# Optimization experiments

Measured on AMD Instinct MI355X. Metric: run time of the kernel, lower is better.

Reference implementation:

```python
import jax, jax.numpy as jnp
import numpy as np

KERNEL_SIZE = 15  # module init kwarg


def _box_filter(x, k):
    c = x.shape[1]
    dn = ('NCHW', 'OIHW', 'NCHW')
    kh = jnp.ones((c, 1, k, 1), x.dtype)
    kw = jnp.ones((c, 1, 1, k), x.dtype)
    p = k // 2
    x = jax.lax.conv_general_dilated(x, kh, (1, 1), [(p, p), (0, 0)],
                                     dimension_numbers=dn, feature_group_count=c)
    x = jax.lax.conv_general_dilated(x, kw, (1, 1), [(0, 0), (p, p)],
                                     dimension_numbers=dn, feature_group_count=c)
    return x


def setup_inputs() -> dict:
    key = jax.random.key(0)
    k1, k2 = jax.random.split(key)
    b, c, h, w = 8, 19, 512, 1024
    input = jax.random.normal(k1, (b, c, h, w), dtype=jnp.float32)
    target = jax.random.randint(k2, (b, 1, h, w), 0, c, dtype=jnp.int32)
    return {"input": input, "target": target}


def reference(input, target):
    k = KERNEL_SIZE
    c = input.shape[1]
    # one-hot mask [b,c,h,w] (equivalent to the per-class (target==i) cat loop)
    mask = jnp.transpose(jax.nn.one_hot(target[:, 0], c, dtype=input.dtype), (0, 3, 1, 2))
    # per-class local count of same-class pixels in a k x k window
    count = _box_filter(mask, k)
    # since mask is one-hot, sum over channels picks the count at the true class (>= 1)
    wsum = jnp.sum(count * mask, axis=1, keepdims=True)  # [b,1,h,w]
    weight = (k * k) / wsum
    # gather the input score at the true class and weight it
    out = jnp.sum(input * mask, axis=1, keepdims=True) * (-weight)
    return jnp.mean(out)
```

## Files before the change

kernel.cpp:

```cpp
#include <hip/hip_runtime.h>
#include <stdint.h>

#define BB 8
#define CC 19
#define HH 512
#define WW 1024
#define KK 15
#define RR 7
#define TH 8
#define NROWS (TH + 2*RR)
#define P_DW 34
#define HW (HH*WW)
#define NPIX (BB*HH*WW)
#define NBLK (BB*(HH/TH))

__global__ __launch_bounds__(256) void wce_main(const float* __restrict__ in,
                                                const int* __restrict__ tg,
                                                float* __restrict__ part) {
  __shared__ uint32_t P[CC][NROWS][P_DW];
  __shared__ uint32_t Cc[TH][256];
  __shared__ float wpart[4];
  const int tid = threadIdx.x;
  const int blk = blockIdx.x;
  const int bb  = blk >> 6;
  const int h0  = (blk & 63) * TH;

  uint32_t* pflat = &P[0][0][0];
  #pragma unroll 4
  for (int i = tid; i < CC*NROWS*P_DW; i += 256) pflat[i] = 0;
  __syncthreads();

  for (int idx = tid; idx < NROWS*256; idx += 256) {
    const int r = idx >> 8, d = idx & 255;
    const int h = h0 - RR + r;
    if (h >= 0 && h < HH) {
      const int4 t4 = *reinterpret_cast<const int4*>(&tg[(bb*HH + h)*WW + d*4]);
      const int rc = r - RR;
      if (rc >= 0 && rc < TH)
        Cc[rc][d] = (uint32_t)(t4.x & 0xff)        | ((uint32_t)(t4.y & 0xff) << 8)
                  | ((uint32_t)(t4.z & 0xff) << 16) | ((uint32_t)(t4.w & 0xff) << 24);
      const int col = d * 4;
      const int dw  = 1 + (col >> 5);
      const int b   = col & 31;
      atomicOr(&P[t4.x][r][dw], 1u << (b + 0));
      atomicOr(&P[t4.y][r][dw], 1u << (b + 1));
      atomicOr(&P[t4.z][r][dw], 1u << (b + 2));
      atomicOr(&P[t4.w][r][dw], 1u << (b + 3));
    }
  }
  __syncthreads();

  const int g = tid;
  float acc = 0.0f;

  #define GATHER(s_, c4_, v0_, v1_, v2_, v3_) do {                              \
    (c4_) = Cc[(s_)][g];                                                        \
    const int b_ = bb*CC*HW + (h0 + (s_))*WW + 4*g;                             \
    (v0_) = in[b_ + (int)( (c4_)        & 0xff)*HW + 0];                        \
    (v1_) = in[b_ + (int)(((c4_) >> 8)  & 0xff)*HW + 1];                        \
    (v2_) = in[b_ + (int)(((c4_) >> 16) & 0xff)*HW + 2];                        \
    (v3_) = in[b_ + (int)(((c4_) >> 24) & 0xff)*HW + 3];                        \
  } while (0)

  #define WINDOW(s_, c4_, v0_, v1_, v2_, v3_) do {                              \
    float xv[4] = { (v0_), (v1_), (v2_), (v3_) };                               \
    _Pragma("unroll")                                                           \
    for (int i = 0; i < 4; ++i) {                                               \
      const int c  = (int)(((c4_) >> (8*i)) & 0xff);                            \
      const int lb = 4*g + i - 7;                                               \
      const int q  = (lb >> 5) + 1;                                             \
      const int sh = lb & 31;                                                   \
      const uint32_t* pr = &P[c][(s_)][q];                                      \
      int cn = 0;                                                               \
      _Pragma("unroll")                                                         \
      for (int wr = 0; wr < KK; ++wr) {                                         \
        const uint32_t lo = pr[0], hi = pr[1];                                  \
        cn += __popc(__builtin_amdgcn_alignbit(hi, lo, sh) & 0x7fffu);          \
        pr += P_DW;                                                             \
      }                                                                         \
      acc += xv[i] * (225.0f / (float)cn);                                      \
    }                                                                           \
  } while (0)

  uint32_t c4a, c4b;
  float a0, a1, a2, a3, b0, b1, b2, b3;
  GATHER(0, c4a, a0, a1, a2, a3);

  #pragma unroll 1
  for (int s = 0; s < TH; s += 2) {
    GATHER(s + 1, c4b, b0, b1, b2, b3);
    WINDOW(s, c4a, a0, a1, a2, a3);
    const int s2 = (s + 2 < TH) ? s + 2 : s;
    GATHER(s2, c4a, a0, a1, a2, a3);
    WINDOW(s + 1, c4b, b0, b1, b2, b3);
  }
  #undef GATHER
  #undef WINDOW

  #pragma unroll
  for (int off = 32; off > 0; off >>= 1) acc += __shfl_down(acc, off, 64);
  const int lane = tid & 63, wv = tid >> 6;
  if (lane == 0) wpart[wv] = acc;
  __syncthreads();
  if (tid == 0) part[blk] = wpart[0] + wpart[1] + wpart[2] + wpart[3];
}

__global__ __launch_bounds__(256) void wce_reduce(const float* __restrict__ part,
                                                  float* __restrict__ out, int n) {
  __shared__ float wpart[4];
  float a = 0.0f;
  for (int i = threadIdx.x; i < n; i += 256) a += part[i];
  #pragma unroll
  for (int off = 32; off > 0; off >>= 1) a += __shfl_down(a, off, 64);
  const int lane = threadIdx.x & 63, wv = threadIdx.x >> 6;
  if (lane == 0) wpart[wv] = a;
  __syncthreads();
  if (threadIdx.x == 0) {
    const float tot = wpart[0] + wpart[1] + wpart[2] + wpart[3];
    out[0] = -tot / (float)NPIX;
  }
}

extern "C" void kernel_launch(void* const* d_in, const int* in_sizes, int n_in,
                              void* d_out, int out_size, void* d_ws, size_t ws_size,
                              hipStream_t stream) {
  const float* in = (const float*)d_in[0];
  const int*   tg = (const int*)d_in[1];
  float* out  = (float*)d_out;
  float* part = (float*)d_ws;

  wce_main<<<NBLK, 256, 0, stream>>>(in, tg, part);
  wce_reduce<<<1, 256, 0, stream>>>(part, out, NBLK);
}
```

Measured before the change: 53.03 us.

## Split each row tile into two width halves to double block count

Each block now covers an 8-row by 512-column tile with a 16-column halo instead of the full 1024-wide row band, doubling the grid to 1024 blocks. The shared-memory bitmask shrinks to 18 dwords per row, and each thread handles 4 of the 8 output rows for its 4 columns. The aim is more blocks and less LDS per block for better occupancy and load balance. The cost is redundant halo target loads, bitmask construction work, and a wider reduction partial array.

```diff
diff --git a/kernel.cpp b/kernel.cpp
--- a/kernel.cpp
+++ b/kernel.cpp
@@ -8,40 +8,45 @@
 #define KK 15
 #define RR 7
 #define TH 8
+#define WHALF 512
 #define NROWS (TH + 2*RR)
-#define P_DW 34
+#define P_DW 18
+#define NK 136
 #define HW (HH*WW)
 #define NPIX (BB*HH*WW)
-#define NBLK (BB*(HH/TH))
+#define NBLK (BB*(HH/TH)*2)
 
 __global__ __launch_bounds__(256) void wce_main(const float* __restrict__ in,
                                                 const int* __restrict__ tg,
                                                 float* __restrict__ part) {
   __shared__ uint32_t P[CC][NROWS][P_DW];
-  __shared__ uint32_t Cc[TH][256];
+  __shared__ uint32_t Cc[TH][WHALF/4];
   __shared__ float wpart[4];
   const int tid = threadIdx.x;
   const int blk = blockIdx.x;
-  const int bb  = blk >> 6;
-  const int h0  = (blk & 63) * TH;
+  const int bb  = blk >> 7;
+  const int rem = blk & 127;
+  const int h0  = (rem >> 1) * TH;
+  const int w0  = (rem & 1) * WHALF;
 
   uint32_t* pflat = &P[0][0][0];
   #pragma unroll 4
   for (int i = tid; i < CC*NROWS*P_DW; i += 256) pflat[i] = 0;
   __syncthreads();
 
-  for (int idx = tid; idx < NROWS*256; idx += 256) {
-    const int r = idx >> 8, d = idx & 255;
+  for (int idx = tid; idx < NROWS*NK; idx += 256) {
+    const int r = idx / NK;
+    const int k = idx - r*NK;
     const int h = h0 - RR + r;
-    if (h >= 0 && h < HH) {
-      const int4 t4 = *reinterpret_cast<const int4*>(&tg[(bb*HH + h)*WW + d*4]);
+    const int wg = w0 - 16 + 4*k;
+    if (h >= 0 && h < HH && wg >= 0 && wg < WW) {
+      const int4 t4 = *reinterpret_cast<const int4*>(&tg[(bb*HH + h)*WW + wg]);
       const int rc = r - RR;
-      if (rc >= 0 && rc < TH)
-        Cc[rc][d] = (uint32_t)(t4.x & 0xff)        | ((uint32_t)(t4.y & 0xff) << 8)
-                  | ((uint32_t)(t4.z & 0xff) << 16) | ((uint32_t)(t4.w & 0xff) << 24);
-      const int col = d * 4;
-      const int dw  = 1 + (col >> 5);
-      const int b   = col & 31;
+      if (rc >= 0 && rc < TH && k >= 4 && k < 132)
+        Cc[rc][k-4] = (uint32_t)(t4.x & 0xff)        | ((uint32_t)(t4.y & 0xff) << 8)
+                    | ((uint32_t)(t4.z & 0xff) << 16) | ((uint32_t)(t4.w & 0xff) << 24);
+      const int dw = k >> 3;
+      const int b  = (4*k) & 31;
       atomicOr(&P[t4.x][r][dw], 1u << (b + 0));
       atomicOr(&P[t4.y][r][dw], 1u << (b + 1));
       atomicOr(&P[t4.z][r][dw], 1u << (b + 2));
@@ -50,12 +55,13 @@
   }
   __syncthreads();
 
-  const int g = tid;
+  const int g  = tid & 127;
+  const int sb = (tid >> 7) << 2;
   float acc = 0.0f;
 
   #define GATHER(s_, c4_, v0_, v1_, v2_, v3_) do {                              \
     (c4_) = Cc[(s_)][g];                                                        \
-    const int b_ = bb*CC*HW + (h0 + (s_))*WW + 4*g;                             \
+    const int b_ = bb*CC*HW + (h0 + (s_))*WW + w0 + 4*g;                        \
     (v0_) = in[b_ + (int)( (c4_)        & 0xff)*HW + 0];                        \
     (v1_) = in[b_ + (int)(((c4_) >> 8)  & 0xff)*HW + 1];                        \
     (v2_) = in[b_ + (int)(((c4_) >> 16) & 0xff)*HW + 2];                        \
@@ -67,8 +73,8 @@
     _Pragma("unroll")                                                           \
     for (int i = 0; i < 4; ++i) {                                               \
       const int c  = (int)(((c4_) >> (8*i)) & 0xff);                            \
-      const int lb = 4*g + i - 7;                                               \
-      const int q  = (lb >> 5) + 1;                                             \
+      const int lb = 4*g + i + 9;              \
+      const int q  = lb >> 5;                                                   \
       const int sh = lb & 31;                                                   \
       const uint32_t* pr = &P[c][(s_)][q];                                      \
       int cn = 0;                                                               \
@@ -78,19 +84,19 @@
         cn += __popc(__builtin_amdgcn_alignbit(hi, lo, sh) & 0x7fffu);          \
         pr += P_DW;                                                             \
       }                                                                         \
-      acc += xv[i] * (225.0f / (float)cn);                                      \
+      acc += xv[i] * (225.0f / (float)cn);        \
     }                                                                           \
   } while (0)
 
   uint32_t c4a, c4b;
   float a0, a1, a2, a3, b0, b1, b2, b3;
-  GATHER(0, c4a, a0, a1, a2, a3);
+  GATHER(sb, c4a, a0, a1, a2, a3);
 
   #pragma unroll 1
-  for (int s = 0; s < TH; s += 2) {
+  for (int s = sb; s < sb + 4; s += 2) {
     GATHER(s + 1, c4b, b0, b1, b2, b3);
     WINDOW(s, c4a, a0, a1, a2, a3);
-    const int s2 = (s + 2 < TH) ? s + 2 : s;
+    const int s2 = (s + 2 < sb + 4) ? s + 2 : s;
     GATHER(s2, c4a, a0, a1, a2, a3);
     WINDOW(s + 1, c4b, b0, b1, b2, b3);
   }
```

Measured after the change: 56.20 us. 1.06x slower.
